# Performance work log

Measured on AMD Instinct MI355X. Metric: run time of the kernel, lower is better.

The kernel has to match this reference:

```python
import jax, jax.numpy as jnp
import numpy as np

BLKPT = 1.0     # black-point percentile
WHTPT = 99.0    # white-point percentile
MAX_MULT = 1.5  # cap on brightening multiplier


def setup_inputs() -> dict:
    key = jax.random.key(0)
    # [B, 3, H, W] image in [0, 1]
    image = jax.random.uniform(key, (16, 3, 1024, 1024), dtype=jnp.float32)
    # standard BT.601 RGB->YUV matrix (module buffer RGB2YUV)
    rgb2yuv = jnp.array([[0.299, 0.587, 0.114],
                         [-0.14713, -0.28886, 0.436],
                         [0.615, -0.51499, -0.10001]], dtype=jnp.float32)
    return {"image": image, "rgb2yuv": rgb2yuv}


def reference(image, rgb2yuv):
    # Only the Y (luma) channel of the YUV conversion is consumed, so we
    # contract with the first matrix row instead of materializing full YUV.
    y = jnp.einsum('j,bjhw->bhw', rgb2yuv[0], image)        # [B, H, W]
    yf = y.reshape(y.shape[0], -1)                          # [B, H*W]
    blkpt = jnp.percentile(yf, BLKPT, axis=1)               # [B]
    whtpt = jnp.percentile(yf, WHTPT, axis=1)               # [B]
    mult = jnp.minimum(1.0 / (whtpt - blkpt), MAX_MULT)     # max_mult > 0 branch
    blkpt = blkpt[:, None, None, None]
    mult = mult[:, None, None, None]
    return jnp.clip((image - blkpt) * mult, 0.0, 1.0)
```

## Files before the change

### kernel.cpp

```cpp
#include <hip/hip_runtime.h>

#define NPIX (1024 * 1024)
#define NBATCH 16
#define NBINS 8192
#define SUBPB 32
#define HTHREADS 512

typedef float vfloat4 __attribute__((ext_vector_type(4)));

__global__ void zero_kernel(unsigned int* __restrict__ g, int n) {
    int i = blockIdx.x * blockDim.x + threadIdx.x;
    for (; i < n; i += gridDim.x * blockDim.x) g[i] = 0u;
}

__global__ __launch_bounds__(HTHREADS) void hist_kernel(
        const float* __restrict__ img,
        const float* __restrict__ rgb2yuv,
        unsigned int* __restrict__ ghist,
        unsigned int* __restrict__ flags,
        float* __restrict__ stats) {
    __shared__ unsigned int lh[NBINS];
    __shared__ unsigned int segsum[HTHREADS];
    __shared__ float vals[4];
    __shared__ int isLast;

    for (int i = threadIdx.x; i < NBINS; i += HTHREADS) lh[i] = 0;
    const float c0 = rgb2yuv[0];
    const float c1 = rgb2yuv[1];
    const float c2 = rgb2yuv[2];
    __syncthreads();

    const int b = blockIdx.x / SUBPB;
    const int s = blockIdx.x % SUBPB;
    const int pixPerBlock = NPIX / SUBPB;
    const size_t base = (size_t)b * 3 * NPIX + (size_t)s * pixPerBlock;

    const float4* r4 = (const float4*)(img + base);
    const float4* g4 = (const float4*)(img + base + NPIX);
    const float4* b4 = (const float4*)(img + base + 2 * (size_t)NPIX);
    const int n4 = pixPerBlock / 4;

    const float scale = (float)NBINS;
    for (int i = threadIdx.x; i < n4; i += HTHREADS) {
        float4 R = r4[i];
        float4 G = g4[i];
        float4 B = b4[i];
        float y0 = c0 * R.x + c1 * G.x + c2 * B.x;
        float y1 = c0 * R.y + c1 * G.y + c2 * B.y;
        float y2 = c0 * R.z + c1 * G.z + c2 * B.z;
        float y3 = c0 * R.w + c1 * G.w + c2 * B.w;
        int i0 = min(NBINS - 1, max(0, (int)(y0 * scale)));
        int i1 = min(NBINS - 1, max(0, (int)(y1 * scale)));
        int i2 = min(NBINS - 1, max(0, (int)(y2 * scale)));
        int i3 = min(NBINS - 1, max(0, (int)(y3 * scale)));
        atomicAdd(&lh[i0], 1u);
        atomicAdd(&lh[i1], 1u);
        atomicAdd(&lh[i2], 1u);
        atomicAdd(&lh[i3], 1u);
    }
    __syncthreads();

    unsigned int* dst = ghist + (size_t)b * NBINS;
    for (int i = threadIdx.x; i < NBINS; i += HTHREADS) {
        unsigned int v = lh[i];
        if (v) atomicAdd(&dst[i], v);
    }

    __threadfence();
    if (threadIdx.x == 0) {
        unsigned int old = atomicAdd(&flags[b], 1u);
        isLast = (old == SUBPB - 1u) ? 1 : 0;
    }
    __syncthreads();
    if (!isLast) return;
    __threadfence();

    const int t = threadIdx.x;
    const uint4* gh = (const uint4*)(ghist + (size_t)b * NBINS);
    uint4* lh4 = (uint4*)lh;
    unsigned int ss = 0;
#pragma unroll
    for (int k = 0; k < 4; ++k) {
        uint4 h = gh[t * 4 + k];
        lh4[t * 4 + k] = h;
        ss += h.x + h.y + h.z + h.w;
    }
    segsum[t] = ss;
    __syncthreads();

    for (int off = 1; off < HTHREADS; off <<= 1) {
        unsigned int v = segsum[t];
        unsigned int add = (t >= off) ? segsum[t - off] : 0u;
        __syncthreads();
        segsum[t] = v + add;
        __syncthreads();
    }

    const unsigned int cumincl = segsum[t];
    const unsigned int cumbefore = (t > 0) ? segsum[t - 1] : 0u;

    const unsigned int ranks[4] = {10485u, 10486u, 1038089u, 1038090u};
    const int BPT = NBINS / HTHREADS;
#pragma unroll
    for (int q = 0; q < 4; ++q) {
        unsigned int r = ranks[q];
        if (r >= cumbefore && r < cumincl) {
            unsigned int running = cumbefore;
            for (int j = 0; j < BPT; ++j) {
                unsigned int c = lh[t * BPT + j];
                if (r < running + c) {
                    float v = ((float)(t * BPT + j) +
                               ((float)(r - running) + 0.5f) / (float)c) *
                              (1.0f / (float)NBINS);
                    vals[q] = v;
                    break;
                }
                running += c;
            }
        }
    }
    __syncthreads();

    if (t == 0) {
        float blk = 0.25f * vals[0] + 0.75f * vals[1];
        float wht = 0.75f * vals[2] + 0.25f * vals[3];
        float mult = fminf(1.0f / (wht - blk), 1.5f);
        stats[b * 2 + 0] = blk;
        stats[b * 2 + 1] = mult;
    }
}

__global__ __launch_bounds__(256) void apply_kernel(
        const float* __restrict__ img,
        const float* __restrict__ stats,
        float* __restrict__ out) {
    const int blocksPerBatch = (3 * NPIX / 4) / 1024;
    const int b = blockIdx.x / blocksPerBatch;
    const int c = blockIdx.x % blocksPerBatch;
    const float blk = stats[b * 2 + 0];
    const float mult = stats[b * 2 + 1];

    const vfloat4* in4 =
        (const vfloat4*)(img + (size_t)b * 3 * NPIX) + (size_t)c * 1024;
    vfloat4* out4 = (vfloat4*)(out + (size_t)b * 3 * NPIX) + (size_t)c * 1024;

#pragma unroll
    for (int i = 0; i < 4; ++i) {
        int idx = i * 256 + threadIdx.x;
        vfloat4 v = in4[idx];
        v.x = fminf(fmaxf((v.x - blk) * mult, 0.0f), 1.0f);
        v.y = fminf(fmaxf((v.y - blk) * mult, 0.0f), 1.0f);
        v.z = fminf(fmaxf((v.z - blk) * mult, 0.0f), 1.0f);
        v.w = fminf(fmaxf((v.w - blk) * mult, 0.0f), 1.0f);
        out4[idx] = v;
    }
}

extern "C" void kernel_launch(void* const* d_in, const int* in_sizes, int n_in,
                              void* d_out, int out_size, void* d_ws, size_t ws_size,
                              hipStream_t stream) {
    const float* img = (const float*)d_in[0];
    const float* rgb2yuv = (const float*)d_in[1];
    float* out = (float*)d_out;

    float* stats = (float*)d_ws;
    unsigned int* ghist = (unsigned int*)((char*)d_ws + 256);
    unsigned int* flags = ghist + NBATCH * NBINS;

    zero_kernel<<<512, 256, 0, stream>>>(ghist, NBATCH * NBINS + NBATCH);
    hist_kernel<<<NBATCH * SUBPB, HTHREADS, 0, stream>>>(img, rgb2yuv, ghist,
                                                         flags, stats);
    const int applyBlocks = NBATCH * ((3 * NPIX / 4) / 1024);
    apply_kernel<<<applyBlocks, 256, 0, stream>>>(img, stats, out);
}
```

Before: 454.2 us.

## Fuse zero, histogram, percentile and apply into one cooperative kernel

Replaces the three launches (zero, histogram, apply) with a single cooperative kernel that uses grid-wide syncs between the phases. The first sixteen blocks compute each batch's percentiles, then every block applies the normalisation to the same slice it histogrammed. The histogram loop is also unrolled to two float4 loads per channel per iteration. This removes launch overhead and the last-block flag scheme, at the cost of three grid barriers and a 512-block apply phase with less parallelism than the earlier apply grid.

```diff
diff --git a/kernel.cpp b/kernel.cpp
--- a/kernel.cpp
+++ b/kernel.cpp
@@ -1,158 +1,171 @@
 #include <hip/hip_runtime.h>
+#include <hip/hip_cooperative_groups.h>
+
+namespace cg = cooperative_groups;
 
 #define NPIX (1024 * 1024)
 #define NBATCH 16
 #define NBINS 8192
-#define SUBPB 32
-#define HTHREADS 512
+#define GRID 512
+#define THREADS 512
+#define SUBPB (GRID / NBATCH)
+#define PIXPB (NPIX / SUBPB)
 
 typedef float vfloat4 __attribute__((ext_vector_type(4)));
 
-__global__ void zero_kernel(unsigned int* __restrict__ g, int n) {
-    int i = blockIdx.x * blockDim.x + threadIdx.x;
-    for (; i < n; i += gridDim.x * blockDim.x) g[i] = 0u;
-}
-
-__global__ __launch_bounds__(HTHREADS) void hist_kernel(
+__global__ __launch_bounds__(THREADS) void fused_kernel(
         const float* __restrict__ img,
         const float* __restrict__ rgb2yuv,
         unsigned int* __restrict__ ghist,
-        unsigned int* __restrict__ flags,
-        float* __restrict__ stats) {
+        float* __restrict__ stats,
+        float* __restrict__ out) {
     __shared__ unsigned int lh[NBINS];
-    __shared__ unsigned int segsum[HTHREADS];
+    __shared__ unsigned int segsum[THREADS];
     __shared__ float vals[4];
-    __shared__ int isLast;
 
-    for (int i = threadIdx.x; i < NBINS; i += HTHREADS) lh[i] = 0;
+    cg::grid_group grid = cg::this_grid();
+    const int t = threadIdx.x;
+    const int blk = blockIdx.x;
+    const int b = blk / SUBPB;
+    const int s = blk % SUBPB;
+
+    {
+        int gtid = blk * THREADS + t;
+        if (gtid < NBATCH * NBINS) ghist[gtid] = 0u;
+        for (int i = t; i < NBINS; i += THREADS) lh[i] = 0u;
+    }
     const float c0 = rgb2yuv[0];
     const float c1 = rgb2yuv[1];
     const float c2 = rgb2yuv[2];
-    __syncthreads();
+    grid.sync();
 
-    const int b = blockIdx.x / SUBPB;
-    const int s = blockIdx.x % SUBPB;
-    const int pixPerBlock = NPIX / SUBPB;
-    const size_t base = (size_t)b * 3 * NPIX + (size_t)s * pixPerBlock;
+    {
+        const size_t base = (size_t)b * 3 * NPIX + (size_t)s * PIXPB;
+        const float4* r4 = (const float4*)(img + base);
+        const float4* g4 = (const float4*)(img + base + NPIX);
+        const float4* b4 = (const float4*)(img + base + 2 * (size_t)NPIX);
+        const int n4 = PIXPB / 4;
+        const float scale = (float)NBINS;
 
-    const float4* r4 = (const float4*)(img + base);
-    const float4* g4 = (const float4*)(img + base + NPIX);
-    const float4* b4 = (const float4*)(img + base + 2 * (size_t)NPIX);
-    const int n4 = pixPerBlock / 4;
+        for (int i = t; i < n4; i += 2 * THREADS) {
+            float4 R0 = r4[i];
+            float4 R1 = r4[i + THREADS];
+            float4 G0 = g4[i];
+            float4 G1 = g4[i + THREADS];
+            float4 B0 = b4[i];
+            float4 B1 = b4[i + THREADS];
 
-    const float scale = (float)NBINS;
-    for (int i = threadIdx.x; i < n4; i += HTHREADS) {
-        float4 R = r4[i];
-        float4 G = g4[i];
-        float4 B = b4[i];
-        float y0 = c0 * R.x + c1 * G.x + c2 * B.x;
-        float y1 = c0 * R.y + c1 * G.y + c2 * B.y;
-        float y2 = c0 * R.z + c1 * G.z + c2 * B.z;
-        float y3 = c0 * R.w + c1 * G.w + c2 * B.w;
-        int i0 = min(NBINS - 1, max(0, (int)(y0 * scale)));
-        int i1 = min(NBINS - 1, max(0, (int)(y1 * scale)));
-        int i2 = min(NBINS - 1, max(0, (int)(y2 * scale)));
-        int i3 = min(NBINS - 1, max(0, (int)(y3 * scale)));
-        atomicAdd(&lh[i0], 1u);
-        atomicAdd(&lh[i1], 1u);
-        atomicAdd(&lh[i2], 1u);
-        atomicAdd(&lh[i3], 1u);
+            float y0 = c0 * R0.x + c1 * G0.x + c2 * B0.x;
+            float y1 = c0 * R0.y + c1 * G0.y + c2 * B0.y;
+            float y2 = c0 * R0.z + c1 * G0.z + c2 * B0.z;
+            float y3 = c0 * R0.w + c1 * G0.w + c2 * B0.w;
+            float y4 = c0 * R1.x + c1 * G1.x + c2 * B1.x;
+            float y5 = c0 * R1.y + c1 * G1.y + c2 * B1.y;
+            float y6 = c0 * R1.z + c1 * G1.z + c2 * B1.z;
+            float y7 = c0 * R1.w + c1 * G1.w + c2 * B1.w;
+
+            int i0 = min(NBINS - 1, max(0, (int)(y0 * scale)));
+            int i1 = min(NBINS - 1, max(0, (int)(y1 * scale)));
+            int i2 = min(NBINS - 1, max(0, (int)(y2 * scale)));
+            int i3 = min(NBINS - 1, max(0, (int)(y3 * scale)));
+            int i4 = min(NBINS - 1, max(0, (int)(y4 * scale)));
+            int i5 = min(NBINS - 1, max(0, (int)(y5 * scale)));
+            int i6 = min(NBINS - 1, max(0, (int)(y6 * scale)));
+            int i7 = min(NBINS - 1, max(0, (int)(y7 * scale)));
+
+            atomicAdd(&lh[i0], 1u);
+            atomicAdd(&lh[i1], 1u);
+            atomicAdd(&lh[i2], 1u);
+            atomicAdd(&lh[i3], 1u);
+            atomicAdd(&lh[i4], 1u);
+            atomicAdd(&lh[i5], 1u);
+            atomicAdd(&lh[i6], 1u);
+            atomicAdd(&lh[i7], 1u);
+        }
+        __syncthreads();
+
+        unsigned int* dst = ghist + (size_t)b * NBINS;
+        for (int i = t; i < NBINS; i += THREADS) {
+            unsigned int v = lh[i];
+            if (v) atomicAdd(&dst[i], v);
+        }
+        __threadfence();
     }
-    __syncthreads();
+    grid.sync();
 
-    unsigned int* dst = ghist + (size_t)b * NBINS;
-    for (int i = threadIdx.x; i < NBINS; i += HTHREADS) {
-        unsigned int v = lh[i];
-        if (v) atomicAdd(&dst[i], v);
-    }
+    if (blk < NBATCH) {
+        const uint4* gh = (const uint4*)(ghist + (size_t)blk * NBINS);
+        uint4* lh4 = (uint4*)lh;
+        unsigned int ss = 0;
+#pragma unroll
+        for (int k = 0; k < 4; ++k) {
+            uint4 h = gh[t * 4 + k];
+            lh4[t * 4 + k] = h;
+            ss += h.x + h.y + h.z + h.w;
+        }
+        segsum[t] = ss;
+        __syncthreads();
 
-    __threadfence();
-    if (threadIdx.x == 0) {
-        unsigned int old = atomicAdd(&flags[b], 1u);
-        isLast = (old == SUBPB - 1u) ? 1 : 0;
-    }
-    __syncthreads();
-    if (!isLast) return;
-    __threadfence();
+        for (int off = 1; off < THREADS; off <<= 1) {
+            unsigned int v = segsum[t];
+            unsigned int add = (t >= off) ? segsum[t - off] : 0u;
+            __syncthreads();
+            segsum[t] = v + add;
+            __syncthreads();
+        }
 
-    const int t = threadIdx.x;
-    const uint4* gh = (const uint4*)(ghist + (size_t)b * NBINS);
-    uint4* lh4 = (uint4*)lh;
-    unsigned int ss = 0;
+        const unsigned int cumincl = segsum[t];
+        const unsigned int cumbefore = (t > 0) ? segsum[t - 1] : 0u;
+
+        const unsigned int ranks[4] = {10485u, 10486u, 1038089u, 1038090u};
+        const int BPT = NBINS / THREADS;
 #pragma unroll
-    for (int k = 0; k < 4; ++k) {
-        uint4 h = gh[t * 4 + k];
-        lh4[t * 4 + k] = h;
-        ss += h.x + h.y + h.z + h.w;
-    }
-    segsum[t] = ss;
-    __syncthreads();
-
-    for (int off = 1; off < HTHREADS; off <<= 1) {
-        unsigned int v = segsum[t];
-        unsigned int add = (t >= off) ? segsum[t - off] : 0u;
-        __syncthreads();
-        segsum[t] = v + add;
-        __syncthreads();
-    }
-
-    const unsigned int cumincl = segsum[t];
-    const unsigned int cumbefore = (t > 0) ? segsum[t - 1] : 0u;
-
-    const unsigned int ranks[4] = {10485u, 10486u, 1038089u, 1038090u};
-    const int BPT = NBINS / HTHREADS;
-#pragma unroll
-    for (int q = 0; q < 4; ++q) {
-        unsigned int r = ranks[q];
-        if (r >= cumbefore && r < cumincl) {
-            unsigned int running = cumbefore;
-            for (int j = 0; j < BPT; ++j) {
-                unsigned int c = lh[t * BPT + j];
-                if (r < running + c) {
-                    float v = ((float)(t * BPT + j) +
-                               ((float)(r - running) + 0.5f) / (float)c) *
-                              (1.0f / (float)NBINS);
-                    vals[q] = v;
-                    break;
+        for (int q = 0; q < 4; ++q) {
+            unsigned int r = ranks[q];
+            if (r >= cumbefore && r < cumincl) {
+                unsigned int running = cumbefore;
+                for (int j = 0; j < BPT; ++j) {
+                    unsigned int c = lh[t * BPT + j];
+                    if (r < running + c) {
+                        vals[q] = ((float)(t * BPT + j) +
+                                   ((float)(r - running) + 0.5f) / (float)c) *
+                                  (1.0f / (float)NBINS);
+                        break;
+                    }
+                    running += c;
                 }
-                running += c;
             }
         }
+        __syncthreads();
+
+        if (t == 0) {
+            float blkp = 0.25f * vals[0] + 0.75f * vals[1];
+            float wht = 0.75f * vals[2] + 0.25f * vals[3];
+            float mult = fminf(1.0f / (wht - blkp), 1.5f);
+            stats[blk * 2 + 0] = blkp;
+            stats[blk * 2 + 1] = mult;
+        }
+        __threadfence();
     }
-    __syncthreads();
+    grid.sync();
 
-    if (t == 0) {
-        float blk = 0.25f * vals[0] + 0.75f * vals[1];
-        float wht = 0.75f * vals[2] + 0.25f * vals[3];
-        float mult = fminf(1.0f / (wht - blk), 1.5f);
-        stats[b * 2 + 0] = blk;
-        stats[b * 2 + 1] = mult;
-    }
-}
+    {
+        const float blkp = stats[b * 2 + 0];
+        const float mult = stats[b * 2 + 1];
+        const int n = 3 * PIXPB / 4;
+        const vfloat4* in4 =
+            (const vfloat4*)(img + (size_t)b * 3 * NPIX) + (size_t)s * n;
+        vfloat4* o4 = (vfloat4*)(out + (size_t)b * 3 * NPIX) + (size_t)s * n;
 
-__global__ __launch_bounds__(256) void apply_kernel(
-        const float* __restrict__ img,
-        const float* __restrict__ stats,
-        float* __restrict__ out) {
-    const int blocksPerBatch = (3 * NPIX / 4) / 1024;
-    const int b = blockIdx.x / blocksPerBatch;
-    const int c = blockIdx.x % blocksPerBatch;
-    const float blk = stats[b * 2 + 0];
-    const float mult = stats[b * 2 + 1];
-
-    const vfloat4* in4 =
-        (const vfloat4*)(img + (size_t)b * 3 * NPIX) + (size_t)c * 1024;
-    vfloat4* out4 = (vfloat4*)(out + (size_t)b * 3 * NPIX) + (size_t)c * 1024;
-
-#pragma unroll
-    for (int i = 0; i < 4; ++i) {
-        int idx = i * 256 + threadIdx.x;
-        vfloat4 v = in4[idx];
-        v.x = fminf(fmaxf((v.x - blk) * mult, 0.0f), 1.0f);
-        v.y = fminf(fmaxf((v.y - blk) * mult, 0.0f), 1.0f);
-        v.z = fminf(fmaxf((v.z - blk) * mult, 0.0f), 1.0f);
-        v.w = fminf(fmaxf((v.w - blk) * mult, 0.0f), 1.0f);
-        out4[idx] = v;
+#pragma unroll 4
+        for (int i = t; i < n; i += THREADS) {
+            vfloat4 v = in4[i];
+            v.x = fminf(fmaxf((v.x - blkp) * mult, 0.0f), 1.0f);
+            v.y = fminf(fmaxf((v.y - blkp) * mult, 0.0f), 1.0f);
+            v.z = fminf(fmaxf((v.z - blkp) * mult, 0.0f), 1.0f);
+            v.w = fminf(fmaxf((v.w - blkp) * mult, 0.0f), 1.0f);
+            o4[i] = v;
+        }
     }
 }
 
@@ -165,11 +178,9 @@
 
     float* stats = (float*)d_ws;
     unsigned int* ghist = (unsigned int*)((char*)d_ws + 256);
-    unsigned int* flags = ghist + NBATCH * NBINS;
 
-    zero_kernel<<<512, 256, 0, stream>>>(ghist, NBATCH * NBINS + NBATCH);
-    hist_kernel<<<NBATCH * SUBPB, HTHREADS, 0, stream>>>(img, rgb2yuv, ghist,
-                                                         flags, stats);
-    const int applyBlocks = NBATCH * ((3 * NPIX / 4) / 1024);
-    apply_kernel<<<applyBlocks, 256, 0, stream>>>(img, stats, out);
+    void* args[] = {(void*)&img, (void*)&rgb2yuv, (void*)&ghist, (void*)&stats,
+                    (void*)&out};
+    hipLaunchCooperativeKernel((void*)fused_kernel, dim3(GRID), dim3(THREADS),
+                               args, 0, stream);
 }
```

New measurement: 643.5 us. 41.7% more time.
